# Kernel tuning notes

Measured on AMD Instinct MI355X. Metric: run time of the kernel, lower is better.

## Reference

```python
import jax, jax.numpy as jnp
import numpy as np

DWT_SCALE = 0.5   # per-tap Haar analysis scale (2D factor = 0.25)
IDWT_SCALE = 1.0  # per-tap Haar synthesis scale (exact inverse of 0.5 analysis)
CONV_PAD = 1      # (kernel_size - 1) // 2 for k = 3


def haar_dwt(x, s):
    # x: [B, C, H, W] -> [B, 4C, H/2, W/2], subband-major: [LL | LH | HL | HH]
    a = x[..., 0::2, 0::2]
    b = x[..., 0::2, 1::2]
    c = x[..., 1::2, 0::2]
    d = x[..., 1::2, 1::2]
    s2 = s * s
    ll = s2 * (a + b + c + d)
    lh = s2 * (a + b - c - d)
    hl = s2 * (a - b + c - d)
    hh = s2 * (a - b - c + d)
    return jnp.concatenate([ll, lh, hl, hh], axis=1)


def haar_idwt(y, t):
    # y: [B, 4C, H2, W2] -> [B, C, 2*H2, 2*W2]; exact inverse of haar_dwt when t*s == 0.5 per tap? (t=1, s=0.5 here)
    B, C4, H2, W2 = y.shape
    C = C4 // 4
    ll, lh, hl, hh = jnp.split(y, 4, axis=1)
    t2 = t * t
    a = t2 * (ll + lh + hl + hh)
    b = t2 * (ll + lh - hl - hh)
    c = t2 * (ll - lh + hl - hh)
    d = t2 * (ll - lh - hl + hh)
    top = jnp.stack([a, b], axis=-1).reshape(B, C, H2, 2 * W2)
    bot = jnp.stack([c, d], axis=-1).reshape(B, C, H2, 2 * W2)
    return jnp.stack([top, bot], axis=-2).reshape(B, C, 2 * H2, 2 * W2)


def conv2d(x, w, stride, pad):
    return jax.lax.conv_general_dilated(
        x, w, (stride, stride), [(pad, pad), (pad, pad)],
        dimension_numbers=('NCHW', 'OIHW', 'NCHW'))


def setup_inputs() -> dict:
    key = jax.random.key(0)
    ks = jax.random.split(key, 5)
    B, C, H, W, K, L = 4, 64, 192, 192, 3, 3
    x = jax.random.normal(ks[0], (B, C, H, W), dtype=jnp.float32)
    # kaiming_uniform_ with a=2.236: bound = sqrt(6 / ((1 + a^2) * fan_in))
    fan_in = 4 * C * K * K
    bound = float(np.sqrt(6.0 / ((1.0 + 2.236 ** 2) * fan_in)))
    inp = {'x': x}
    for i in range(L):
        inp[f'w{i}'] = jax.random.uniform(ks[1 + i], (4 * C, 4 * C, K, K), jnp.float32, -bound, bound)
    inp['bias'] = jnp.zeros((C,), jnp.float32)
    return inp


def reference(x, w0, w1, w2, bias):
    H, W = x.shape[-2:]
    weights = [w0, w1, w2]
    L = len(weights)
    pad_factor = 2 ** L
    pad_h = (-H) % pad_factor
    pad_w = (-W) % pad_factor
    xp = x
    if pad_h > 0 or pad_w > 0:
        xp = jnp.pad(x, ((0, 0), (0, 0), (0, pad_h), (0, pad_w)), mode='reflect')
    # decompose: DWT -> dense conv over stacked subbands; recurse on the conv'd LL band
    curr = xp
    highs = []
    for w in weights:
        d = haar_dwt(curr, DWT_SCALE)          # [B, 4C, H/2, W/2]
        y = conv2d(d, w, 1, CONV_PAD)          # [B, 4C_out, H/2, W/2]
        c_out = w.shape[0] // 4
        curr = y[:, :c_out]                    # LL -> next level
        highs.append(y[:, c_out:])             # LH, HL, HH kept for reconstruction
    # reconstruct bottom-up
    ll = curr
    for h in reversed(highs):
        ll = haar_idwt(jnp.concatenate([ll, h], axis=1), IDWT_SCALE)
    out = ll[..., :H, :W] + bias[None, :, None, None]
    return out
```

## Files before the change

### kernel.cpp

```cpp
#include <hip/hip_runtime.h>
#include <hip/hip_bf16.h>
#include <cstddef>


typedef __attribute__((ext_vector_type(8))) short short8;
typedef __attribute__((ext_vector_type(4))) float f32x4;
typedef __attribute__((ext_vector_type(4))) unsigned short u16x4;

static __device__ __forceinline__ unsigned short f2bf(float f) {
    __hip_bfloat16 h = __float2bfloat16(f);
    return *reinterpret_cast<unsigned short*>(&h);
}
static __device__ __forceinline__ float bf2f(unsigned short u) {
    return __uint_as_float(((unsigned int)u) << 16);
}

static __device__ __forceinline__ void gload_lds16(const short* g, short* l) {
    __builtin_amdgcn_global_load_lds(
        (const __attribute__((address_space(1))) void*)g,
        (__attribute__((address_space(3))) void*)l, 16, 0, 0);
}

__global__ __launch_bounds__(256) void mega_prep_kernel(
    const float* __restrict__ x,
    const float* __restrict__ wa, const float* __restrict__ wb,
    const float* __restrict__ wc,
    unsigned short* __restrict__ ta, unsigned short* __restrict__ tb,
    unsigned short* __restrict__ tc,
    unsigned short* __restrict__ p0, unsigned short* __restrict__ p1,
    unsigned short* __restrict__ p2)
{
    __shared__ float lds[4 * 64 * 17];
    const int bx = blockIdx.x;
    const int tid = threadIdx.x;
    if (bx < 864) {
        const int sel = bx / 288;
        const float* w = (sel == 0) ? wa : (sel == 1) ? wb : wc;
        unsigned short* wT = (sel == 0) ? ta : (sel == 1) ? tb : tc;
        int idx = (bx - sel * 288) * 256 + tid;
        int co = idx & 255;
        int g = (idx >> 8) & 3;
        int kb = (idx >> 10) & 7;
        int tap = idx >> 13;
        int cin0 = kb * 32 + g * 8;
        unsigned short tmp[8];
#pragma unroll
        for (int e = 0; e < 8; ++e)
            tmp[e] = f2bf(w[((size_t)co * 256 + cin0 + e) * 9 + tap]);
        *(short8*)(wT + (size_t)idx * 8) = *(const short8*)tmp;
        return;
    }
    if (bx < 1206) {
        constexpr int N0 = 49664, N1 = 25088, N2 = 12800;
        int idx = (bx - 864) * 256 + tid;
        unsigned short* base; int HP, WP, rel;
        if (idx < N0)           { base = p0; HP = 98; WP = 98; rel = idx; }
        else if (idx < N0 + N1) { base = p1; HP = 50; WP = 50; rel = idx - N0; }
        else                    { base = p2; HP = 26; WP = 26; rel = idx - N0 - N1; }
        int nb = 64 * WP + (HP - 2) * 64;
        int b = rel / nb, r = rel % nb;
        int row, kg, px;
        if (r < 64 * WP) {
            int rowSel = r / (32 * WP), rr = r % (32 * WP);
            kg = rr / WP; px = rr % WP; row = rowSel ? (HP - 1) : 0;
        } else {
            int r2 = r - 64 * WP;
            row = 1 + (r2 >> 6);
            int r3 = r2 & 63;
            kg = r3 >> 1; px = (r3 & 1) ? (WP - 1) : 0;
        }
        size_t o = (((size_t)(b * HP + row) * 32 + kg) * WP + px) * 8;
        short8 z = {};
        *(short8*)(base + o) = z;
        return;
    }
    const int bx2 = bx - 1206;
    const int j0 = (bx2 % 6) * 16;
    const int i  = (bx2 / 6) % 96;
    const int b  = bx2 / 576;
    const int j = tid & 15;
    const int c4 = tid >> 4;
#pragma unroll
    for (int it = 0; it < 4; ++it) {
        int c = c4 + it * 16;
        const float* p = x + ((size_t)(b * 64 + c) * 192 + 2 * i) * 192 + 2 * (j0 + j);
        float2 top = *(const float2*)p;
        float2 bot = *(const float2*)(p + 192);
        float a = top.x, bb = top.y, cc = bot.x, dd = bot.y;
        const float s2 = 0.25f;
        lds[(0 * 64 + c) * 17 + j] = s2 * (a + bb + cc + dd);
        lds[(1 * 64 + c) * 17 + j] = s2 * (a + bb - cc - dd);
        lds[(2 * 64 + c) * 17 + j] = s2 * (a - bb + cc - dd);
        lds[(3 * 64 + c) * 17 + j] = s2 * (a - bb - cc + dd);
    }
    __syncthreads();
#pragma unroll
    for (int it = 0; it < 2; ++it) {
        int idx = it * 256 + tid;
        int jj = idx & 15;
        int g = (idx >> 4) & 3;
        int kb = idx >> 6;
        int sub = kb >> 1;
        int c0 = (kb & 1) * 32 + g * 8;
        unsigned short tmp[8];
#pragma unroll
        for (int e = 0; e < 8; ++e)
            tmp[e] = f2bf(lds[(sub * 64 + c0 + e) * 17 + jj]);
        size_t o = ((((size_t)(b * 98 + 1 + i) * 8 + kb) * 4 + g) * 98 + 1 + j0 + jj) * 8;
        *(short8*)(p0 + o) = *(const short8*)tmp;
    }
}

template <int H2, int JB>
__global__ __launch_bounds__(256) void dwt_mid_kernel(
    const unsigned short* __restrict__ in, unsigned short* __restrict__ Xp)
{
    constexpr int W2 = H2, Wi = 2 * W2, WPn = W2 + 2, HPn = H2 + 2;
    constexpr int LS = JB + 1;
    __shared__ float lds[4 * 64 * LS];
    const int j0 = blockIdx.x * JB;
    const int i = blockIdx.y;
    const int b = blockIdx.z;
    const int tid = threadIdx.x;
    const int c = tid & 63;
    const int jq = tid >> 6;
#pragma unroll
    for (int it = 0; it < JB / 4; ++it) {
        int jl = jq + it * 4;
        int j = j0 + jl;
        const unsigned short* p = in + ((size_t)(b * 2 * H2 + 2 * i) * Wi + 2 * j) * 256 + c;
        float a  = bf2f(p[0]);
        float bb = bf2f(p[256]);
        float cc = bf2f(p[(size_t)Wi * 256]);
        float dd = bf2f(p[(size_t)Wi * 256 + 256]);
        const float s2 = 0.25f;
        lds[(0 * 64 + c) * LS + jl] = s2 * (a + bb + cc + dd);
        lds[(1 * 64 + c) * LS + jl] = s2 * (a + bb - cc - dd);
        lds[(2 * 64 + c) * LS + jl] = s2 * (a - bb + cc - dd);
        lds[(3 * 64 + c) * LS + jl] = s2 * (a - bb - cc + dd);
    }
    __syncthreads();
    constexpr int CH = 8 * 4 * JB;
#pragma unroll
    for (int it = 0; it < (CH + 255) / 256; ++it) {
        int idx = it * 256 + tid;
        if (idx < CH) {
            int jj = idx % JB;
            int g = (idx / JB) & 3;
            int kb = idx / (JB * 4);
            int sub = kb >> 1;
            int c0 = (kb & 1) * 32 + g * 8;
            unsigned short tmp[8];
#pragma unroll
            for (int e = 0; e < 8; ++e)
                tmp[e] = f2bf(lds[(sub * 64 + c0 + e) * LS + jj]);
            size_t o = ((((size_t)(b * HPn + 1 + i) * 8 + kb) * 4 + g) * WPn + 1 + j0 + jj) * 8;
            *(short8*)(Xp + o) = *(const short8*)tmp;
        }
    }
}

template <int HP, int WP, int PR, int PC, int XCHUNK>
__global__ __launch_bounds__(128) void conv_reg_kernel(
    const short* __restrict__ Xp, const short* __restrict__ Wt,
    unsigned short* __restrict__ Y)
{
    constexpr int WN = 2;
    constexpr int NPX = PR * PC;
    constexpr int MFR = 4;
    constexpr int NFR = NPX / (16 * WN);
    constexpr int RPF = 16 / PC;
    constexpr int BROWS = (NFR - 1) * RPF + 3;
    constexpr int H = HP - 2, W = WP - 2;
    constexpr int rowT = H / PR, colT = W / PC;
    constexpr int PH = PR + 2, PW = PC + 2;
    constexpr int RAW = PH * PW;
    constexpr int SLOTG = (RAW + 63) & ~63;
    constexpr int TI = 4 * SLOTG / 64;
    constexpr int TIW = TI / WN;
    constexpr size_t S_r = (size_t)256 * WP;
    constexpr size_t S_kb = (size_t)32 * WP;
    constexpr size_t S_g = (size_t)8 * WP;

    __shared__ __align__(16) short bufA[4 * SLOTG * 8];
    __shared__ __align__(16) short bufB[4 * SLOTG * 8];

    int bid = blockIdx.x;
    if (XCHUNK > 0) bid = (bid & 7) * XCHUNK + (bid >> 3);
    const int tx = bid % colT; bid /= colT;
    const int ty = bid % rowT; bid /= rowT;
    const int b = bid;
    const int gy0 = ty * PR;
    const int gx0 = tx * PC;
    const int cb = blockIdx.y * 64;

    const int lane = threadIdx.x & 63;
    const int wn = threadIdx.x >> 6;
    const int n15 = lane & 15, gq = lane >> 4;

    const size_t bBase = (size_t)(b * HP + gy0) * S_r + (size_t)gx0 * 8;

    size_t sSrc[TIW]; int sDst[TIW];
#pragma unroll
    for (int ti = 0; ti < TIW; ++ti) {
        int t = wn * TIW + ti;
        int d = t * 64 + lane;
        int g = d / SLOTG;
        int p = d - g * SLOTG;
        int prow = p / PW, pcol = p - prow * PW;
        sDst[ti] = d * 8;
        sSrc[ti] = (p < RAW)
            ? bBase + (size_t)prow * S_r + (size_t)g * S_g + (size_t)pcol * 8
            : bBase;
    }

    const short* aBase = Wt + (size_t)gq * 2048 + (size_t)(cb + n15) * 8;
    const int rB = wn * (PR / WN) + n15 / PC;
    const int cB = n15 % PC;
    const int bSlot = gq * SLOTG + rB * PW + cB;

    f32x4 acc[MFR][NFR] = {};
    short8 a[9][MFR];

    auto stage = [&](int kbv, short* dBuf) {
#pragma unroll
        for (int ti = 0; ti < TIW; ++ti)
            gload_lds16(Xp + sSrc[ti] + (size_t)kbv * S_kb, dBuf + sDst[ti]);
    };
    auto ldA = [&](int tap, int kbv, int m) -> short8 {
        return *(const short8*)(aBase + (size_t)tap * 65536
                                + (size_t)kbv * 8192 + m * 128);
    };

    stage(0, bufA);
#pragma unroll
    for (int s = 0; s < 9; ++s)
#pragma unroll
        for (int m = 0; m < MFR; ++m)
            a[s][m] = ldA(s, 0, m);
    asm volatile("s_waitcnt vmcnt(0)" ::: "memory");
    __builtin_amdgcn_sched_barrier(0);
    __builtin_amdgcn_s_barrier();

    auto kbBody = [&](int kb, const short* cur, short* nxt) {
        const int kbn = (kb < 7) ? kb + 1 : 7;
        stage(kbn, nxt);
        __builtin_amdgcn_sched_barrier(0);
        short8 Br[BROWS][3];
#pragma unroll
        for (int r = 0; r < BROWS; ++r)
#pragma unroll
            for (int kx = 0; kx < 3; ++kx)
                Br[r][kx] = *(const short8*)(cur + (bSlot + r * PW + kx) * 8);
#pragma unroll
        for (int s = 0; s < 9; ++s) {
            const int ky = s / 3, kx = s - 3 * (s / 3);
            __builtin_amdgcn_s_setprio(1);
#pragma unroll
            for (int m = 0; m < MFR; ++m)
#pragma unroll
                for (int n = 0; n < NFR; ++n)
                    acc[m][n] = __builtin_amdgcn_mfma_f32_16x16x32_bf16(
                        a[s][m], Br[n * RPF + ky][kx], acc[m][n], 0, 0, 0);
            __builtin_amdgcn_s_setprio(0);
#pragma unroll
            for (int m = 0; m < MFR; ++m)
                a[s][m] = ldA(s, kbn, m);
        }
        __builtin_amdgcn_sched_barrier(0);
        asm volatile("s_waitcnt vmcnt(36)" ::: "memory");
        __builtin_amdgcn_sched_barrier(0);
        __builtin_amdgcn_s_barrier();
    };

#pragma unroll 1
    for (int u = 0; u < 4; ++u) {
        kbBody(2 * u, bufA, bufB);
        kbBody(2 * u + 1, bufB, bufA);
    }

#pragma unroll
    for (int m = 0; m < MFR; ++m)
#pragma unroll
        for (int n = 0; n < NFR; ++n) {
            int cout = cb + m * 16 + gq * 4;
            int row = wn * (PR / WN) + n * RPF + n15 / PC;
            int col = n15 % PC;
            unsigned short* op = Y + ((size_t)(b * H + gy0 + row) * W + gx0 + col) * 256 + cout;
            u16x4 sv;
#pragma unroll
            for (int q = 0; q < 4; ++q) sv[q] = f2bf(acc[m][n][q]);
            *(u16x4*)op = sv;
        }
}

__global__ __launch_bounds__(256) void idwt_fused_kernel(
    const unsigned short* __restrict__ y2, const unsigned short* __restrict__ y1,
    const unsigned short* __restrict__ y0h,
    const float* __restrict__ bias, float* __restrict__ out)
{
    __shared__ float lds[16 * 324];
    const int tt = blockIdx.x;
    const int tyi = tt / 12, txi = tt % 12;
    const int y0 = tyi * 8, x0 = txi * 8;
    const int cg = blockIdx.y;
    const int b = blockIdx.z;
    const int tid = threadIdx.x;

#pragma unroll
    for (int rep = 0; rep < 4; ++rep) {
        int idx = rep * 256 + tid;
        int c16 = idx & 15;
        int px = idx >> 4;
        int pi = px >> 3, pj = px & 7;
        int c = cg * 16 + c16;
        int pi96 = y0 + pi, pj96 = x0 + pj;
        int pi48 = pi96 >> 1, pj48 = pj96 >> 1;
        int pi24 = pi48 >> 1, pj24 = pj48 >> 1;
        const unsigned short* h2 = y2 + ((size_t)(b * 24 + pi24) * 24 + pj24) * 256;
        float l2   = bf2f(h2[c]);
        float l2lh = bf2f(h2[64 + c]);
        float l2hl = bf2f(h2[128 + c]);
        float l2hh = bf2f(h2[192 + c]);
        float s1 = 1.f - 2.f * (pi48 & 1), t1 = 1.f - 2.f * (pj48 & 1);
        float ll1v = l2 + s1 * l2lh + t1 * l2hl + (s1 * t1) * l2hh;
        const unsigned short* h1 = y1 + ((size_t)(b * 48 + pi48) * 48 + pj48) * 256;
        float l1lh = bf2f(h1[64 + c]);
        float l1hl = bf2f(h1[128 + c]);
        float l1hh = bf2f(h1[192 + c]);
        float s0 = 1.f - 2.f * (pi96 & 1), t0 = 1.f - 2.f * (pj96 & 1);
        float vll = ll1v + s0 * l1lh + t0 * l1hl + (s0 * t0) * l1hh;
        const unsigned short* hp = y0h + ((size_t)(b * 96 + pi96) * 96 + pj96) * 256;
        float vlh = bf2f(hp[64 + c]);
        float vhl = bf2f(hp[128 + c]);
        float vhh = bf2f(hp[192 + c]);
        float bv = bias[c];
        float a  = vll + vlh + vhl + vhh + bv;
        float b2 = vll + vlh - vhl - vhh + bv;
        float c2 = vll - vlh + vhl - vhh + bv;
        float d2 = vll - vlh - vhl + vhh + bv;
        float* l = lds + c16 * 324 + (2 * pi) * 20 + 2 * pj;
        l[0] = a; l[1] = b2;
        l[20] = c2; l[21] = d2;
    }
    __syncthreads();

    const int c16 = tid >> 4;
    const int yy = tid & 15;
    const float* l = lds + c16 * 324 + yy * 20;
    float* op = out + ((size_t)(b * 64 + cg * 16 + c16) * 192 + tyi * 16 + yy) * 192 + txi * 16;
#pragma unroll
    for (int q = 0; q < 4; ++q)
        *(f32x4*)(op + 4 * q) = *(const f32x4*)(l + 4 * q);
}

extern "C" void kernel_launch(void* const* d_in, const int* in_sizes, int n_in,
                              void* d_out, int out_size, void* d_ws, size_t ws_size,
                              hipStream_t stream)
{
    const float* x    = (const float*)d_in[0];
    const float* w0   = (const float*)d_in[1];
    const float* w1   = (const float*)d_in[2];
    const float* w2   = (const float*)d_in[3];
    const float* bias = (const float*)d_in[4];
    float* out = (float*)d_out;

    char* ws = (char*)d_ws;
    unsigned short* wT0 = (unsigned short*)(ws + 0);
    unsigned short* wT1 = (unsigned short*)(ws + 1179648);
    unsigned short* wT2 = (unsigned short*)(ws + 2359296);
    unsigned short* Xp0 = (unsigned short*)(ws + 3538944);
    unsigned short* Xp1 = (unsigned short*)(ws + 23207936);
    unsigned short* Xp2 = (unsigned short*)(ws + 28327936);
    unsigned short* y0 = (unsigned short*)(ws + 29712384);
    unsigned short* y1 = (unsigned short*)(ws + 48586752);
    unsigned short* y2 = (unsigned short*)(ws + 53305344);

    mega_prep_kernel<<<3510, 256, 0, stream>>>(x, w0, w1, w2, wT0, wT1, wT2,
                                               Xp0, Xp1, Xp2);

    conv_reg_kernel<98, 98, 4, 16, 72><<<dim3(576, 4), 128, 0, stream>>>(
        (const short*)Xp0, (const short*)wT0, y0);

    dwt_mid_kernel<48, 16><<<dim3(3, 48, 4), 256, 0, stream>>>(y0, Xp1);
    conv_reg_kernel<50, 50, 4, 16, 18><<<dim3(144, 4), 128, 0, stream>>>(
        (const short*)Xp1, (const short*)wT1, y1);

    dwt_mid_kernel<24, 12><<<dim3(2, 24, 4), 256, 0, stream>>>(y1, Xp2);
    conv_reg_kernel<26, 26, 4, 8, 9><<<dim3(72, 4), 128, 0, stream>>>(
        (const short*)Xp2, (const short*)wT2, y2);

    idwt_fused_kernel<<<dim3(144, 4, 4), 256, 0, stream>>>(y2, y1, y0, bias, out);
}
```

Measured before the change: 145.5 us.

## Stage full input tile in LDS once and rotate weight prefetch ring

Replaces the double-buffered per-k-block LDS staging with a single up-front load of all 8 k-blocks of the input tile into LDS, which removes the per-iteration barriers. Tiles shrink to 4x8 pixels with one N-fragment per wave, so the grid doubles for the first two levels. Weight fragments now sit in a 6-slot rotating register ring that prefetches six taps ahead, and B fragments are double-buffered in registers. Each block does less MFMA work per weight load, so weight traffic rises, while occupancy and latency hiding improve.

After: 182.0 us. +25.1%, slower.

```diff
diff --git a/kernel.cpp b/kernel.cpp
--- a/kernel.cpp
+++ b/kernel.cpp
@@ -160,30 +160,23 @@
     }
 }
 
-template <int HP, int WP, int PR, int PC, int XCHUNK>
-__global__ __launch_bounds__(128) void conv_reg_kernel(
+template <int HP, int WP, int XCHUNK>
+__global__ __launch_bounds__(128) void conv_full_kernel(
     const short* __restrict__ Xp, const short* __restrict__ Wt,
     unsigned short* __restrict__ Y)
 {
-    constexpr int WN = 2;
-    constexpr int NPX = PR * PC;
-    constexpr int MFR = 4;
-    constexpr int NFR = NPX / (16 * WN);
-    constexpr int RPF = 16 / PC;
-    constexpr int BROWS = (NFR - 1) * RPF + 3;
+    constexpr int PR = 4, PC = 8, MFR = 4;
     constexpr int H = HP - 2, W = WP - 2;
     constexpr int rowT = H / PR, colT = W / PC;
     constexpr int PH = PR + 2, PW = PC + 2;
     constexpr int RAW = PH * PW;
-    constexpr int SLOTG = (RAW + 63) & ~63;
-    constexpr int TI = 4 * SLOTG / 64;
-    constexpr int TIW = TI / WN;
+    constexpr int SLOT = (RAW + 63) & ~63;
+    constexpr int TIW = 16;
     constexpr size_t S_r = (size_t)256 * WP;
     constexpr size_t S_kb = (size_t)32 * WP;
     constexpr size_t S_g = (size_t)8 * WP;
 
-    __shared__ __align__(16) short bufA[4 * SLOTG * 8];
-    __shared__ __align__(16) short bufB[4 * SLOTG * 8];
+    __shared__ __align__(16) short lsB[8 * 4 * SLOT * 8];
 
     int bid = blockIdx.x;
     if (XCHUNK > 0) bid = (bid & 7) * XCHUNK + (bid >> 3);
@@ -200,98 +193,93 @@
 
     const size_t bBase = (size_t)(b * HP + gy0) * S_r + (size_t)gx0 * 8;
 
-    size_t sSrc[TIW]; int sDst[TIW];
 #pragma unroll
     for (int ti = 0; ti < TIW; ++ti) {
-        int t = wn * TIW + ti;
-        int d = t * 64 + lane;
-        int g = d / SLOTG;
-        int p = d - g * SLOTG;
-        int prow = p / PW, pcol = p - prow * PW;
-        sDst[ti] = d * 8;
-        sSrc[ti] = (p < RAW)
-            ? bBase + (size_t)prow * S_r + (size_t)g * S_g + (size_t)pcol * 8
+        int d = (wn * TIW + ti) * 64 + lane;
+        int kb = d >> 8;
+        int r = d & 255;
+        int g = r >> 6;
+        int slot = r & 63;
+        int prow = slot / PW, pcol = slot % PW;
+        size_t src = (slot < RAW)
+            ? bBase + (size_t)prow * S_r + (size_t)kb * S_kb
+              + (size_t)g * S_g + (size_t)pcol * 8
             : bBase;
+        gload_lds16(Xp + src, &lsB[(size_t)d * 8]);
     }
 
     const short* aBase = Wt + (size_t)gq * 2048 + (size_t)(cb + n15) * 8;
-    const int rB = wn * (PR / WN) + n15 / PC;
+    const int rB = wn * 2 + n15 / PC;
     const int cB = n15 % PC;
-    const int bSlot = gq * SLOTG + rB * PW + cB;
-
-    f32x4 acc[MFR][NFR] = {};
-    short8 a[9][MFR];
-
-    auto stage = [&](int kbv, short* dBuf) {
-#pragma unroll
-        for (int ti = 0; ti < TIW; ++ti)
-            gload_lds16(Xp + sSrc[ti] + (size_t)kbv * S_kb, dBuf + sDst[ti]);
-    };
+    const int bSlot = gq * SLOT + rB * PW + cB;
+
+    f32x4 acc[MFR] = {};
+    short8 a[6][MFR];
+    short8 BrA[3][3], BrB[3][3];
+
     auto ldA = [&](int tap, int kbv, int m) -> short8 {
         return *(const short8*)(aBase + (size_t)tap * 65536
                                 + (size_t)kbv * 8192 + m * 128);
     };
-
-    stage(0, bufA);
-#pragma unroll
-    for (int s = 0; s < 9; ++s)
+    auto ldBr = [&](int kbv, short8 (*Br)[3]) {
+#pragma unroll
+        for (int ky = 0; ky < 3; ++ky)
+#pragma unroll
+            for (int kx = 0; kx < 3; ++kx)
+                Br[ky][kx] = *(const short8*)&lsB[
+                    (size_t)(kbv * 256 + bSlot + ky * PW + kx) * 8];
+    };
+
+#pragma unroll
+    for (int s = 0; s < 6; ++s)
 #pragma unroll
         for (int m = 0; m < MFR; ++m)
             a[s][m] = ldA(s, 0, m);
+
     asm volatile("s_waitcnt vmcnt(0)" ::: "memory");
     __builtin_amdgcn_sched_barrier(0);
     __builtin_amdgcn_s_barrier();
 
-    auto kbBody = [&](int kb, const short* cur, short* nxt) {
+    ldBr(0, BrA);
+
+    auto kbBody = [&](int kb, int P, short8 (*cur)[3], short8 (*nxt)[3]) {
         const int kbn = (kb < 7) ? kb + 1 : 7;
-        stage(kbn, nxt);
-        __builtin_amdgcn_sched_barrier(0);
-        short8 Br[BROWS][3];
-#pragma unroll
-        for (int r = 0; r < BROWS; ++r)
-#pragma unroll
-            for (int kx = 0; kx < 3; ++kx)
-                Br[r][kx] = *(const short8*)(cur + (bSlot + r * PW + kx) * 8);
+        ldBr(kbn, nxt);
 #pragma unroll
         for (int s = 0; s < 9; ++s) {
-            const int ky = s / 3, kx = s - 3 * (s / 3);
+            const int ky = s / 3, kx = s - 3 * ky;
+            const int rs = (3 * P + s) % 6;
             __builtin_amdgcn_s_setprio(1);
 #pragma unroll
             for (int m = 0; m < MFR; ++m)
-#pragma unroll
-                for (int n = 0; n < NFR; ++n)
-                    acc[m][n] = __builtin_amdgcn_mfma_f32_16x16x32_bf16(
-                        a[s][m], Br[n * RPF + ky][kx], acc[m][n], 0, 0, 0);
+                acc[m] = __builtin_amdgcn_mfma_f32_16x16x32_bf16(
+                    a[rs][m], cur[ky][kx], acc[m], 0, 0, 0);
             __builtin_amdgcn_s_setprio(0);
+            const int ftap = (s + 6 < 9) ? s + 6 : s - 3;
+            const int fkb  = (s + 6 < 9) ? kb : kbn;
 #pragma unroll
             for (int m = 0; m < MFR; ++m)
-                a[s][m] = ldA(s, kbn, m);
+                a[rs][m] = ldA(ftap, fkb, m);
         }
-        __builtin_amdgcn_sched_barrier(0);
-        asm volatile("s_waitcnt vmcnt(36)" ::: "memory");
-        __builtin_amdgcn_sched_barrier(0);
-        __builtin_amdgcn_s_barrier();
     };
 
 #pragma unroll 1
     for (int u = 0; u < 4; ++u) {
-        kbBody(2 * u, bufA, bufB);
-        kbBody(2 * u + 1, bufB, bufA);
-    }
-
-#pragma unroll
-    for (int m = 0; m < MFR; ++m)
-#pragma unroll
-        for (int n = 0; n < NFR; ++n) {
-            int cout = cb + m * 16 + gq * 4;
-            int row = wn * (PR / WN) + n * RPF + n15 / PC;
-            int col = n15 % PC;
-            unsigned short* op = Y + ((size_t)(b * H + gy0 + row) * W + gx0 + col) * 256 + cout;
-            u16x4 sv;
-#pragma unroll
-            for (int q = 0; q < 4; ++q) sv[q] = f2bf(acc[m][n][q]);
-            *(u16x4*)op = sv;
-        }
+        kbBody(2 * u,     0, BrA, BrB);
+        kbBody(2 * u + 1, 1, BrB, BrA);
+    }
+
+#pragma unroll
+    for (int m = 0; m < MFR; ++m) {
+        int cout = cb + m * 16 + gq * 4;
+        int row = gy0 + rB;
+        int col = gx0 + cB;
+        unsigned short* op = Y + ((size_t)(b * H + row) * W + col) * 256 + cout;
+        u16x4 sv;
+#pragma unroll
+        for (int q = 0; q < 4; ++q) sv[q] = f2bf(acc[m][q]);
+        *(u16x4*)op = sv;
+    }
 }
 
 __global__ __launch_bounds__(256) void idwt_fused_kernel(
@@ -379,15 +367,15 @@
     mega_prep_kernel<<<3510, 256, 0, stream>>>(x, w0, w1, w2, wT0, wT1, wT2,
                                                Xp0, Xp1, Xp2);
 
-    conv_reg_kernel<98, 98, 4, 16, 72><<<dim3(576, 4), 128, 0, stream>>>(
+    conv_full_kernel<98, 98, 144><<<dim3(1152, 4), 128, 0, stream>>>(
         (const short*)Xp0, (const short*)wT0, y0);
 
     dwt_mid_kernel<48, 16><<<dim3(3, 48, 4), 256, 0, stream>>>(y0, Xp1);
-    conv_reg_kernel<50, 50, 4, 16, 18><<<dim3(144, 4), 128, 0, stream>>>(
+    conv_full_kernel<50, 50, 36><<<dim3(288, 4), 128, 0, stream>>>(
         (const short*)Xp1, (const short*)wT1, y1);
 
     dwt_mid_kernel<24, 12><<<dim3(2, 24, 4), 256, 0, stream>>>(y1, Xp2);
-    conv_reg_kernel<26, 26, 4, 8, 9><<<dim3(72, 4), 128, 0, stream>>>(
+    conv_full_kernel<26, 26, 9><<<dim3(72, 4), 128, 0, stream>>>(
         (const short*)Xp2, (const short*)wT2, y2);
 
     idwt_fused_kernel<<<dim3(144, 4, 4), 256, 0, stream>>>(y2, y1, y0, bias, out);
```
